# Kernel optimization log

Measured on AMD Instinct MI355X. Metric: run time of the kernel, lower is better.

## Reference

```python
import jax, jax.numpy as jnp
import numpy as np

IN_DIM = 256
OUT_DIM = 256
EMBED_DIM = 256
GROUPS = 8
BN_EPS = 1e-5


def conv2d(x, w, b, pad, groups=1):
    # x: NCHW, w: OIHW (I = in_ch / groups)
    out = jax.lax.conv_general_dilated(
        x, w, window_strides=(1, 1), padding=[(pad, pad), (pad, pad)],
        dimension_numbers=('NCHW', 'OIHW', 'NCHW'), feature_group_count=groups)
    return out + b[None, :, None, None]


def setup_inputs() -> dict:
    key = jax.random.key(0)
    ks = jax.random.split(key, 8)
    s = 0.05
    d = {}
    d['x'] = jax.random.normal(ks[0], (2, IN_DIM, 16, 16), jnp.float32)
    d['y'] = jax.random.normal(ks[1], (2, OUT_DIM, 128, 128), jnp.float32)
    # channle_reduce: Conv2d(256, 64, k=3, groups=64) -> weight (64, 4, 3, 3)
    d['w_cr'] = jax.random.normal(ks[2], (IN_DIM // 4, 4, 3, 3), jnp.float32) * s
    d['b_cr'] = jnp.zeros((IN_DIM // 4,), jnp.float32)
    # depthwise convs on 64 channels
    d['w_dw3'] = jax.random.normal(ks[3], (IN_DIM // 4, 1, 3, 3), jnp.float32) * s
    d['b_dw3'] = jnp.zeros((IN_DIM // 4,), jnp.float32)
    d['w_dw7'] = jax.random.normal(ks[4], (IN_DIM // 4, 1, 5, 5), jnp.float32) * s
    d['b_dw7'] = jnp.zeros((IN_DIM // 4,), jnp.float32)
    # gate: Conv2d(256, 128, 1) + BN + StarReLU
    d['w_gate'] = jax.random.normal(ks[5], (IN_DIM // 2, IN_DIM, 1, 1), jnp.float32) * s
    d['b_gate'] = jnp.zeros((IN_DIM // 2,), jnp.float32)
    d['bn_gamma'] = jnp.ones((IN_DIM // 2,), jnp.float32)
    d['bn_beta'] = jnp.zeros((IN_DIM // 2,), jnp.float32)
    d['bn_mean'] = jnp.zeros((IN_DIM // 2,), jnp.float32)
    d['bn_var'] = jnp.ones((IN_DIM // 2,), jnp.float32)
    d['sr_scale'] = jnp.ones((1,), jnp.float32)
    d['sr_bias'] = jnp.zeros((1,), jnp.float32)
    # linear1: Linear(16, 8192) -> torch weight shape (8192, 16)
    d['w_lin'] = jax.random.normal(ks[6], (OUT_DIM * EMBED_DIM // GROUPS, IN_DIM // (2 * GROUPS)), jnp.float32) * s
    d['b_lin'] = jnp.zeros((OUT_DIM * EMBED_DIM // GROUPS,), jnp.float32)
    return d


def reference(x, y, w_cr, b_cr, w_dw3, b_dw3, w_dw7, b_dw7, w_gate, b_gate,
              bn_gamma, bn_beta, bn_mean, bn_var, sr_scale, sr_bias, w_lin, b_lin):
    B, C, H, Wd = x.shape
    # gate branch: 1x1 conv -> BN (inference stats) -> StarReLU
    g = conv2d(x, w_gate, b_gate, 0)
    inv = (bn_gamma / jnp.sqrt(bn_var + BN_EPS))[None, :, None, None]
    g = (g - bn_mean[None, :, None, None]) * inv + bn_beta[None, :, None, None]
    g = sr_scale * jnp.square(jnp.maximum(g, 0.0)) + sr_bias
    # feature branch
    xr = conv2d(x, w_cr, b_cr, 1, groups=IN_DIM // 4)        # (B, 64, H, W)
    x3 = conv2d(xr, w_dw3, b_dw3, 1, groups=IN_DIM // 4)
    x7 = conv2d(xr, w_dw7, b_dw7, 2, groups=IN_DIM // 4)
    xc = jnp.concatenate([x3, x7], axis=1) * g               # (B, 128, H, W)
    # per-pixel weight generation: (B,H,W,G,16) @ (16,8192)
    xc = xc.reshape(B, GROUPS, -1, H, Wd).transpose(0, 3, 4, 1, 2)
    wdec = jnp.einsum('bhwgi,oi->bhwgo', xc, w_lin) + b_lin  # (B,H,W,8,8192)
    # flatten (G, out*embed/G) -> (embed, out); matches torch reshape order
    wdec = wdec.reshape(B, H, Wd, EMBED_DIM, OUT_DIM)
    # patch-wise dynamic 1x1 conv == per-patch batched matmul
    b, c, h, w = y.shape
    fh, fw = H, Wd
    ph, pw = h // fh, w // fw
    yp = y.reshape(b, c, fh, ph, fw, pw)
    # out[b,e,f,p,g,q] = sum_c wdec[b,f,g,e,c] * y[b,c,f,p,g,q]
    out = jnp.einsum('bfgec,bcfpgq->befpgq', wdec, yp)
    return out.reshape(b, EMBED_DIM, h, w)
```

## Files before the change

kernel.cpp:

```cpp
#include <hip/hip_runtime.h>
#include <stdint.h>


typedef __attribute__((ext_vector_type(8))) short short8;
typedef __attribute__((ext_vector_type(4))) float f32x4;

#define BN_EPS 1e-5f

__device__ __forceinline__ unsigned short f2bf(float f) {
  unsigned u = __float_as_uint(f);
  return (unsigned short)((u + 0x8000u) >> 16);
}
__device__ __forceinline__ unsigned pk2bf(float a, float b) {
  unsigned ua = __float_as_uint(a), ub = __float_as_uint(b);
  return ((ua + 0x8000u) >> 16) | ((ub + 0x8000u) & 0xFFFF0000u);
}

__global__ __launch_bounds__(256) void k1_merged(
    const float* __restrict__ x, const float* __restrict__ w_cr,
    const float* __restrict__ b_cr, const float* __restrict__ w_dw3,
    const float* __restrict__ b_dw3, const float* __restrict__ w_dw7,
    const float* __restrict__ b_dw7, const float* __restrict__ w_gate,
    const float* __restrict__ b_gate, const float* __restrict__ bn_gamma,
    const float* __restrict__ bn_beta, const float* __restrict__ bn_mean,
    const float* __restrict__ bn_var, const float* __restrict__ sr_scale,
    const float* __restrict__ sr_bias, const float* __restrict__ w_lin,
    short* __restrict__ wlin_bf, float* __restrict__ f0_out,
    float* __restrict__ gs_out)
{
  __shared__ __align__(16) float xcen[256];
  __shared__ __align__(16) float xs[4][256];
  __shared__ __align__(16) float xrs[256];

  int blk = blockIdx.x;
  int t = threadIdx.x;

  if (blk < 512) {
    int b = blk >> 8, h = (blk >> 4) & 15, w = blk & 15;
    int pix = (b * 16 + h) * 16 + w;

    { int idx = blk * 256 + t; wlin_bf[idx] = (short)f2bf(w_lin[idx]); }

    xcen[t] = x[b * 65536 + t * 256 + h * 16 + w];
    __syncthreads();

    int wave = t >> 6, lane = t & 63;
    int oq = lane >> 2, ol = lane & 3;
    const float4* wg4 = (const float4*)w_gate;
    const float4* xc4 = (const float4*)xcen;
    float ss = sr_scale[0], sb = sr_bias[0];

    #pragma unroll
    for (int pass = 0; pass < 2; ++pass) {
      int o = wave * 32 + pass * 16 + oq;
      float acc = 0.f;
      #pragma unroll
      for (int k = 0; k < 16; ++k) {
        int j = k * 4 + ol;
        float4 wv = wg4[o * 64 + j];
        float4 xv = xc4[j];
        acc += wv.x * xv.x + wv.y * xv.y + wv.z * xv.z + wv.w * xv.w;
      }
      acc += __shfl_xor(acc, 1);
      acc += __shfl_xor(acc, 2);
      float inv = bn_gamma[o] * rsqrtf(bn_var[o] + BN_EPS);
      float gg = (acc + b_gate[o] - bn_mean[o]) * inv + bn_beta[o];
      gg = fmaxf(gg, 0.f);
      gg = ss * gg * gg + sb;
      if (ol == 0) gs_out[pix * 128 + o] = gg;
    }
  } else {
    int cb = blk - 512;
    int b = cb >> 6, cr = cb & 63;
    {
      int ch = t >> 6, off = (t & 63) * 4;
      float4 v = *(const float4*)(x + b * 65536 + (cr * 4 + ch) * 256 + off);
      *(float4*)&xs[ch][off] = v;
    }
    __syncthreads();
    int h = t >> 4, w = t & 15;
    float a = b_cr[cr];
    #pragma unroll
    for (int ii = 0; ii < 4; ++ii) {
      const float* wp = w_cr + (cr * 4 + ii) * 9;
      #pragma unroll
      for (int ky = 0; ky < 3; ++ky) {
        int gy = h + ky - 1;
        #pragma unroll
        for (int kx = 0; kx < 3; ++kx) {
          int gx = w + kx - 1;
          float v = (gy >= 0 && gy < 16 && gx >= 0 && gx < 16) ? xs[ii][gy * 16 + gx] : 0.f;
          a += wp[ky * 3 + kx] * v;
        }
      }
    }
    xrs[t] = a;
    __syncthreads();

    float f3 = b_dw3[cr];
    {
      const float* wp = w_dw3 + cr * 9;
      #pragma unroll
      for (int ky = 0; ky < 3; ++ky) {
        int gy = h + ky - 1;
        #pragma unroll
        for (int kx = 0; kx < 3; ++kx) {
          int gx = w + kx - 1;
          float v = (gy >= 0 && gy < 16 && gx >= 0 && gx < 16) ? xrs[gy * 16 + gx] : 0.f;
          f3 += wp[ky * 3 + kx] * v;
        }
      }
    }
    float f5 = b_dw7[cr];
    {
      const float* wp = w_dw7 + cr * 25;
      #pragma unroll
      for (int ky = 0; ky < 5; ++ky) {
        int gy = h + ky - 2;
        #pragma unroll
        for (int kx = 0; kx < 5; ++kx) {
          int gx = w + kx - 2;
          float v = (gy >= 0 && gy < 16 && gx >= 0 && gx < 16) ? xrs[gy * 16 + gx] : 0.f;
          f5 += wp[ky * 5 + kx] * v;
        }
      }
    }
    int pix = (b * 16 + h) * 16 + w;
    f0_out[pix * 128 + cr] = f3;
    f0_out[pix * 128 + 64 + cr] = f5;
  }
}

__global__ __launch_bounds__(512, 4) void k2_fused(
    const float* __restrict__ y, const short* __restrict__ wlin_bf,
    const float* __restrict__ f0_in, const float* __restrict__ gs_in,
    const float* __restrict__ b_lin, float* __restrict__ out)
{
  __shared__ __align__(16) short Ylds[16384];
  __shared__ __align__(16) char dyn[32768];
  float* scratch = (float*)dyn;
  short* wdbuf = (short*)dyn;

  int phys = blockIdx.x;
  int blk = (phys & 7) * 64 + (phys >> 3);
  int b = blk >> 8, f = (blk >> 4) & 15, g = blk & 15;
  int tid = threadIdx.x;
  int wave = tid >> 6, lane = tid & 63;
  int quad = lane >> 4, l16 = lane & 15;
  int geff = l16 & 7, jsel = l16 >> 3;

  const float* yb = y + b * 4194304 + (f * 8) * 128 + g * 8;

  int c32 = tid >> 4, pf = tid & 15;
  float4 yv[4][2];
  #pragma unroll
  for (int sch = 0; sch < 4; ++sch)
    #pragma unroll
    for (int it = 0; it < 2; ++it)
      yv[sch][it] = *(const float4*)(yb + (sch * 64 + it * 32 + c32) * 16384 + (pf >> 1) * 128 + (pf & 1) * 4);

  short8 aw[2][2][2];
  #pragma unroll
  for (int s = 0; s < 2; ++s)
    #pragma unroll
    for (int jj = 0; jj < 2; ++jj) {
      int jA = (wave * 2 + jj) * 2 + (quad >> 1);
      #pragma unroll
      for (int hh = 0; hh < 2; ++hh) {
        int c0 = s * 32 + hh * 16;
        aw[s][jj][hh] = *(const short8*)(wlin_bf + (jA * 256 + c0 + l16) * 16 + (quad & 1) * 8);
      }
    }

  bool bval = (jsel == (quad >> 1));
  const float* fp = f0_in + blk * 128 + geff * 16 + (quad & 1) * 8;
  const float* gp = gs_in + blk * 128 + geff * 16 + (quad & 1) * 8;
  float4 f0a = *(const float4*)fp, f0b = *(const float4*)(fp + 4);
  float4 gsa = *(const float4*)gp, gsb = *(const float4*)(gp + 4);

  #pragma unroll
  for (int sch = 0; sch < 4; ++sch) {
    #pragma unroll
    for (int it = 0; it < 2; ++it)
      *(float4*)&scratch[(it * 32 + c32) * 65 + pf * 4] = yv[sch][it];
    __syncthreads();
    {
      int pix = tid & 63, cg = tid >> 6;
      float s0 = scratch[(cg * 8 + 0) * 65 + pix];
      float s1 = scratch[(cg * 8 + 1) * 65 + pix];
      float s2 = scratch[(cg * 8 + 2) * 65 + pix];
      float s3 = scratch[(cg * 8 + 3) * 65 + pix];
      float s4 = scratch[(cg * 8 + 4) * 65 + pix];
      float s5 = scratch[(cg * 8 + 5) * 65 + pix];
      float s6 = scratch[(cg * 8 + 6) * 65 + pix];
      float s7 = scratch[(cg * 8 + 7) * 65 + pix];
      uint4 pk;
      pk.x = pk2bf(s0, s1); pk.y = pk2bf(s2, s3);
      pk.z = pk2bf(s4, s5); pk.w = pk2bf(s6, s7);
      int chunk = sch * 8 + cg;
      int physc = chunk ^ (pix & 15);
      *(uint4*)&Ylds[pix * 256 + physc * 8] = pk;
    }
    __syncthreads();
  }

  short8 bx = {0, 0, 0, 0, 0, 0, 0, 0};
  if (bval) {
    bx[0] = (short)f2bf(f0a.x * gsa.x); bx[1] = (short)f2bf(f0a.y * gsa.y);
    bx[2] = (short)f2bf(f0a.z * gsa.z); bx[3] = (short)f2bf(f0a.w * gsa.w);
    bx[4] = (short)f2bf(f0b.x * gsb.x); bx[5] = (short)f2bf(f0b.y * gsb.y);
    bx[6] = (short)f2bf(f0b.z * gsb.z); bx[7] = (short)f2bf(f0b.w * gsb.w);
  }

  f32x4 acc[2][4];
  #pragma unroll
  for (int et = 0; et < 2; ++et)
    #pragma unroll
    for (int nt = 0; nt < 4; ++nt)
      acc[et][nt] = {0.f, 0.f, 0.f, 0.f};

  auto gen_chunk = [&](int cc, int buf, int slot) {
    short* dst = wdbuf + buf * 8192;
    #pragma unroll
    for (int jj = 0; jj < 2; ++jj) {
      int jp = wave * 2 + jj;
      int jD = jp * 2 + jsel;
      #pragma unroll
      for (int hh = 0; hh < 2; ++hh) {
        int c0 = cc * 32 + hh * 16;
        float4 bl = *(const float4*)(b_lin + jD * 256 + c0 + quad * 4);
        f32x4 cin = {bl.x, bl.y, bl.z, bl.w};
        f32x4 d = __builtin_amdgcn_mfma_f32_16x16x32_bf16(aw[slot][jj][hh], bx, cin, 0, 0, 0);
        int e = geff * 32 + jD;
        uint2 pk;
        pk.x = pk2bf(d[0], d[1]);
        pk.y = pk2bf(d[2], d[3]);
        int q16 = hh * 2 + (quad >> 1);
        int sw = q16 ^ ((e >> 1) & 3) ^ ((e >> 5) & 3);
        *(uint2*)&dst[e * 32 + sw * 8 + (quad & 1) * 4] = pk;
      }
    }
  };

  gen_chunk(0, 0, 0);
  __syncthreads();

  #pragma unroll
  for (int cc = 0; cc < 8; ++cc) {
    if (cc < 6) {
      #pragma unroll
      for (int jj = 0; jj < 2; ++jj) {
        int jA = (wave * 2 + jj) * 2 + (quad >> 1);
        #pragma unroll
        for (int hh = 0; hh < 2; ++hh) {
          int c0 = (cc + 2) * 32 + hh * 16;
          aw[cc & 1][jj][hh] = *(const short8*)(wlin_bf + (jA * 256 + c0 + l16) * 16 + (quad & 1) * 8);
        }
      }
    }
    if (cc < 7) gen_chunk(cc + 1, (cc + 1) & 1, (cc + 1) & 1);

    const short* src = wdbuf + (cc & 1) * 8192;
    short8 A2[2], Bf[4];
    #pragma unroll
    for (int et = 0; et < 2; ++et) {
      int e = wave * 32 + et * 16 + l16;
      int sw = quad ^ ((e >> 1) & 3) ^ ((e >> 5) & 3);
      A2[et] = *(const short8*)&src[e * 32 + sw * 8];
    }
    int chunkY = cc * 4 + quad;
    #pragma unroll
    for (int nt = 0; nt < 4; ++nt) {
      int physc = chunkY ^ l16;
      Bf[nt] = *(const short8*)&Ylds[(nt * 16 + l16) * 256 + physc * 8];
    }
    #pragma unroll
    for (int et = 0; et < 2; ++et)
      #pragma unroll
      for (int nt = 0; nt < 4; ++nt)
        acc[et][nt] = __builtin_amdgcn_mfma_f32_16x16x32_bf16(A2[et], Bf[nt], acc[et][nt], 0, 0, 0);
    if (cc < 7) __syncthreads();
  }

  float* ob = out + b * 4194304 + (f * 8) * 128 + g * 8;
  #pragma unroll
  for (int et = 0; et < 2; ++et) {
    int e0 = wave * 32 + et * 16 + quad * 4;
    #pragma unroll
    for (int nt = 0; nt < 4; ++nt) {
      int pix = nt * 16 + l16;
      float* oa = ob + (pix >> 3) * 128 + (pix & 7);
      #pragma unroll
      for (int r = 0; r < 4; ++r)
        oa[(e0 + r) * 16384] = acc[et][nt][r];
    }
  }
}

extern "C" void kernel_launch(void* const* d_in, const int* in_sizes, int n_in,
                              void* d_out, int out_size, void* d_ws, size_t ws_size,
                              hipStream_t stream) {
  const float* x        = (const float*)d_in[0];
  const float* y        = (const float*)d_in[1];
  const float* w_cr     = (const float*)d_in[2];
  const float* b_cr     = (const float*)d_in[3];
  const float* w_dw3    = (const float*)d_in[4];
  const float* b_dw3    = (const float*)d_in[5];
  const float* w_dw7    = (const float*)d_in[6];
  const float* b_dw7    = (const float*)d_in[7];
  const float* w_gate   = (const float*)d_in[8];
  const float* b_gate   = (const float*)d_in[9];
  const float* bn_gamma = (const float*)d_in[10];
  const float* bn_beta  = (const float*)d_in[11];
  const float* bn_mean  = (const float*)d_in[12];
  const float* bn_var   = (const float*)d_in[13];
  const float* sr_scale = (const float*)d_in[14];
  const float* sr_bias  = (const float*)d_in[15];
  const float* w_lin    = (const float*)d_in[16];
  const float* b_lin    = (const float*)d_in[17];
  float* out = (float*)d_out;

  float* f0      = (float*)d_ws;
  float* gs      = (float*)((char*)d_ws + 262144);
  short* wlin_bf = (short*)((char*)d_ws + 524288);

  hipLaunchKernelGGL(k1_merged, dim3(640), dim3(256), 0, stream,
                     x, w_cr, b_cr, w_dw3, b_dw3, w_dw7, b_dw7, w_gate, b_gate,
                     bn_gamma, bn_beta, bn_mean, bn_var, sr_scale, sr_bias,
                     w_lin, wlin_bf, f0, gs);
  hipLaunchKernelGGL(k2_fused, dim3(512), dim3(512), 0, stream,
                     y, wlin_bf, f0, gs, b_lin, out);
}
```

Baseline: 153.0 us.

## Split k2 patches in half and make dynamic-weight generation wave-private

Each patch is now split across two blocks (1024 blocks, half the pixels each), which halves LDS use and raises the occupancy target to 8 blocks per CU. The generated dynamic weights are remapped so each wave produces and consumes only its own rows in a private LDS region, which removes the per-chunk block barriers and the double buffer. The y staging transpose is also pipelined with a swizzled scratch layout. In exchange, each block recomputes the same weight-generation MFMAs for its patch, so that work is done twice, and the w_lin fragments are loaded on the fly instead of being prefetched.

```diff
diff --git a/kernel.cpp b/kernel.cpp
--- a/kernel.cpp
+++ b/kernel.cpp
@@ -131,168 +131,152 @@
   }
 }
 
-__global__ __launch_bounds__(512, 4) void k2_fused(
+__global__ __launch_bounds__(512, 8) void k2_fused(
     const float* __restrict__ y, const short* __restrict__ wlin_bf,
     const float* __restrict__ f0_in, const float* __restrict__ gs_in,
     const float* __restrict__ b_lin, float* __restrict__ out)
 {
-  __shared__ __align__(16) short Ylds[16384];
-  __shared__ __align__(16) char dyn[32768];
+  __shared__ __align__(16) short Ylds[8192];
+  __shared__ __align__(16) char dyn[16384];
   float* scratch = (float*)dyn;
-  short* wdbuf = (short*)dyn;
-
+  short* wdbase = (short*)dyn;
+
+  int tid = threadIdx.x;
   int phys = blockIdx.x;
-  int blk = (phys & 7) * 64 + (phys >> 3);
+  int logical = (phys & 7) * 128 + (phys >> 3);
+  int blk = logical >> 1, phalf = logical & 1;
   int b = blk >> 8, f = (blk >> 4) & 15, g = blk & 15;
-  int tid = threadIdx.x;
+
   int wave = tid >> 6, lane = tid & 63;
   int quad = lane >> 4, l16 = lane & 15;
   int geff = l16 & 7, jsel = l16 >> 3;
 
-  const float* yb = y + b * 4194304 + (f * 8) * 128 + g * 8;
-
-  int c32 = tid >> 4, pf = tid & 15;
-  float4 yv[4][2];
-  #pragma unroll
-  for (int sch = 0; sch < 4; ++sch)
-    #pragma unroll
-    for (int it = 0; it < 2; ++it)
-      yv[sch][it] = *(const float4*)(yb + (sch * 64 + it * 32 + c32) * 16384 + (pf >> 1) * 128 + (pf & 1) * 4);
-
-  short8 aw[2][2][2];
-  #pragma unroll
-  for (int s = 0; s < 2; ++s)
-    #pragma unroll
-    for (int jj = 0; jj < 2; ++jj) {
-      int jA = (wave * 2 + jj) * 2 + (quad >> 1);
-      #pragma unroll
-      for (int hh = 0; hh < 2; ++hh) {
-        int c0 = s * 32 + hh * 16;
-        aw[s][jj][hh] = *(const short8*)(wlin_bf + (jA * 256 + c0 + l16) * 16 + (quad & 1) * 8);
-      }
-    }
+  const float* yb = y + b * 4194304 + (f * 8 + phalf * 4) * 128 + g * 8;
+  int cth = tid >> 2, ith = tid & 3;
+
+  float4 yv[2];
+  #pragma unroll
+  for (int j = 0; j < 2; ++j) {
+    int hw = ith * 2 + j;
+    yv[j] = *(const float4*)(yb + cth * 16384 + (hw >> 1) * 128 + (hw & 1) * 4);
+  }
 
   bool bval = (jsel == (quad >> 1));
-  const float* fp = f0_in + blk * 128 + geff * 16 + (quad & 1) * 8;
-  const float* gp = gs_in + blk * 128 + geff * 16 + (quad & 1) * 8;
-  float4 f0a = *(const float4*)fp, f0b = *(const float4*)(fp + 4);
-  float4 gsa = *(const float4*)gp, gsb = *(const float4*)(gp + 4);
-
-  #pragma unroll
-  for (int sch = 0; sch < 4; ++sch) {
-    #pragma unroll
-    for (int it = 0; it < 2; ++it)
-      *(float4*)&scratch[(it * 32 + c32) * 65 + pf * 4] = yv[sch][it];
+  short8 bx = {0, 0, 0, 0, 0, 0, 0, 0};
+  {
+    const float* f0p = f0_in + blk * 128 + geff * 16 + (quad & 1) * 8;
+    const float* gsp = gs_in + blk * 128 + geff * 16 + (quad & 1) * 8;
+    float4 fa = *(const float4*)f0p, fb = *(const float4*)(f0p + 4);
+    float4 ga = *(const float4*)gsp, gb = *(const float4*)(gsp + 4);
+    if (bval) {
+      bx[0] = (short)f2bf(fa.x * ga.x); bx[1] = (short)f2bf(fa.y * ga.y);
+      bx[2] = (short)f2bf(fa.z * ga.z); bx[3] = (short)f2bf(fa.w * ga.w);
+      bx[4] = (short)f2bf(fb.x * gb.x); bx[5] = (short)f2bf(fb.y * gb.y);
+      bx[6] = (short)f2bf(fb.z * gb.z); bx[7] = (short)f2bf(fb.w * gb.w);
+    }
+  }
+
+  #pragma unroll
+  for (int rr = 0; rr < 2; ++rr) {
+    #pragma unroll
+    for (int j = 0; j < 2; ++j) {
+      int hw = ith * 2 + j;
+      *(float4*)&scratch[cth * 32 + ((hw * 4) ^ ((cth & 7) * 4))] = yv[j];
+    }
+    if (rr == 0) {
+      #pragma unroll
+      for (int j = 0; j < 2; ++j) {
+        int hw = ith * 2 + j;
+        yv[j] = *(const float4*)(yb + (128 + cth) * 16384 + (hw >> 1) * 128 + (hw & 1) * 4);
+      }
+    }
     __syncthreads();
     {
-      int pix = tid & 63, cg = tid >> 6;
-      float s0 = scratch[(cg * 8 + 0) * 65 + pix];
-      float s1 = scratch[(cg * 8 + 1) * 65 + pix];
-      float s2 = scratch[(cg * 8 + 2) * 65 + pix];
-      float s3 = scratch[(cg * 8 + 3) * 65 + pix];
-      float s4 = scratch[(cg * 8 + 4) * 65 + pix];
-      float s5 = scratch[(cg * 8 + 5) * 65 + pix];
-      float s6 = scratch[(cg * 8 + 6) * 65 + pix];
-      float s7 = scratch[(cg * 8 + 7) * 65 + pix];
+      int pix = tid & 31, cg = tid >> 5;
+      float s[8];
+      #pragma unroll
+      for (int i2 = 0; i2 < 8; ++i2)
+        s[i2] = scratch[(cg * 8 + i2) * 32 + (pix ^ (i2 * 4))];
       uint4 pk;
-      pk.x = pk2bf(s0, s1); pk.y = pk2bf(s2, s3);
-      pk.z = pk2bf(s4, s5); pk.w = pk2bf(s6, s7);
-      int chunk = sch * 8 + cg;
+      pk.x = pk2bf(s[0], s[1]); pk.y = pk2bf(s[2], s[3]);
+      pk.z = pk2bf(s[4], s[5]); pk.w = pk2bf(s[6], s[7]);
+      int chunk = rr * 16 + cg;
       int physc = chunk ^ (pix & 15);
       *(uint4*)&Ylds[pix * 256 + physc * 8] = pk;
     }
     __syncthreads();
   }
 
-  short8 bx = {0, 0, 0, 0, 0, 0, 0, 0};
-  if (bval) {
-    bx[0] = (short)f2bf(f0a.x * gsa.x); bx[1] = (short)f2bf(f0a.y * gsa.y);
-    bx[2] = (short)f2bf(f0a.z * gsa.z); bx[3] = (short)f2bf(f0a.w * gsa.w);
-    bx[4] = (short)f2bf(f0b.x * gsb.x); bx[5] = (short)f2bf(f0b.y * gsb.y);
-    bx[6] = (short)f2bf(f0b.z * gsb.z); bx[7] = (short)f2bf(f0b.w * gsb.w);
-  }
-
-  f32x4 acc[2][4];
-  #pragma unroll
-  for (int et = 0; et < 2; ++et)
-    #pragma unroll
-    for (int nt = 0; nt < 4; ++nt)
-      acc[et][nt] = {0.f, 0.f, 0.f, 0.f};
-
-  auto gen_chunk = [&](int cc, int buf, int slot) {
-    short* dst = wdbuf + buf * 8192;
+  short* wdw = wdbase + wave * 1024;
+
+  auto gen_chunk = [&](int cc) {
     #pragma unroll
     for (int jj = 0; jj < 2; ++jj) {
-      int jp = wave * 2 + jj;
-      int jD = jp * 2 + jsel;
+      int jD = wave * 4 + jj * 2 + jsel;
+      int jA = wave * 4 + jj * 2 + (quad >> 1);
+      int ep = geff * 4 + jj * 2 + jsel;
+      int gx = ((ep >> 2) & 3) ^ (ep & 3);
       #pragma unroll
       for (int hh = 0; hh < 2; ++hh) {
         int c0 = cc * 32 + hh * 16;
         float4 bl = *(const float4*)(b_lin + jD * 256 + c0 + quad * 4);
         f32x4 cin = {bl.x, bl.y, bl.z, bl.w};
-        f32x4 d = __builtin_amdgcn_mfma_f32_16x16x32_bf16(aw[slot][jj][hh], bx, cin, 0, 0, 0);
-        int e = geff * 32 + jD;
+        short8 aw = *(const short8*)(wlin_bf + (jA * 256 + c0 + l16) * 16 + (quad & 1) * 8);
+        f32x4 d = __builtin_amdgcn_mfma_f32_16x16x32_bf16(aw, bx, cin, 0, 0, 0);
         uint2 pk;
         pk.x = pk2bf(d[0], d[1]);
         pk.y = pk2bf(d[2], d[3]);
-        int q16 = hh * 2 + (quad >> 1);
-        int sw = q16 ^ ((e >> 1) & 3) ^ ((e >> 5) & 3);
-        *(uint2*)&dst[e * 32 + sw * 8 + (quad & 1) * 4] = pk;
+        int q16 = (hh * 2 + (quad >> 1)) ^ gx;
+        *(uint2*)&wdw[ep * 32 + q16 * 8 + (quad & 1) * 4] = pk;
       }
     }
   };
 
-  gen_chunk(0, 0, 0);
-  __syncthreads();
+  f32x4 acc[2][2];
+  #pragma unroll
+  for (int et = 0; et < 2; ++et)
+    #pragma unroll
+    for (int nt = 0; nt < 2; ++nt)
+      acc[et][nt] = {0.f, 0.f, 0.f, 0.f};
+
+  gen_chunk(0);
 
   #pragma unroll
   for (int cc = 0; cc < 8; ++cc) {
-    if (cc < 6) {
-      #pragma unroll
-      for (int jj = 0; jj < 2; ++jj) {
-        int jA = (wave * 2 + jj) * 2 + (quad >> 1);
-        #pragma unroll
-        for (int hh = 0; hh < 2; ++hh) {
-          int c0 = (cc + 2) * 32 + hh * 16;
-          aw[cc & 1][jj][hh] = *(const short8*)(wlin_bf + (jA * 256 + c0 + l16) * 16 + (quad & 1) * 8);
-        }
-      }
-    }
-    if (cc < 7) gen_chunk(cc + 1, (cc + 1) & 1, (cc + 1) & 1);
-
-    const short* src = wdbuf + (cc & 1) * 8192;
-    short8 A2[2], Bf[4];
+    short8 A2[2], Bf[2];
     #pragma unroll
     for (int et = 0; et < 2; ++et) {
-      int e = wave * 32 + et * 16 + l16;
-      int sw = quad ^ ((e >> 1) & 3) ^ ((e >> 5) & 3);
-      A2[et] = *(const short8*)&src[e * 32 + sw * 8];
-    }
-    int chunkY = cc * 4 + quad;
-    #pragma unroll
-    for (int nt = 0; nt < 4; ++nt) {
-      int physc = chunkY ^ l16;
-      Bf[nt] = *(const short8*)&Ylds[(nt * 16 + l16) * 256 + physc * 8];
-    }
+      int ep = (l16 & 7) * 4 + et * 2 + (l16 >> 3);
+      int gx = ((ep >> 2) & 3) ^ (ep & 3);
+      A2[et] = *(const short8*)&wdw[ep * 32 + (quad ^ gx) * 8];
+    }
+    #pragma unroll
+    for (int nt = 0; nt < 2; ++nt) {
+      int pix = nt * 16 + l16;
+      int physc = (cc * 4 + quad) ^ l16;
+      Bf[nt] = *(const short8*)&Ylds[pix * 256 + physc * 8];
+    }
+    if (cc < 7) gen_chunk(cc + 1);
     #pragma unroll
     for (int et = 0; et < 2; ++et)
       #pragma unroll
-      for (int nt = 0; nt < 4; ++nt)
+      for (int nt = 0; nt < 2; ++nt)
         acc[et][nt] = __builtin_amdgcn_mfma_f32_16x16x32_bf16(A2[et], Bf[nt], acc[et][nt], 0, 0, 0);
-    if (cc < 7) __syncthreads();
-  }
-
-  float* ob = out + b * 4194304 + (f * 8) * 128 + g * 8;
+  }
+
+  float* ob = out + b * 4194304 + (f * 8 + phalf * 4) * 128 + g * 8;
   #pragma unroll
   for (int et = 0; et < 2; ++et) {
-    int e0 = wave * 32 + et * 16 + quad * 4;
-    #pragma unroll
-    for (int nt = 0; nt < 4; ++nt) {
+    #pragma unroll
+    for (int nt = 0; nt < 2; ++nt) {
       int pix = nt * 16 + l16;
       float* oa = ob + (pix >> 3) * 128 + (pix & 7);
       #pragma unroll
-      for (int r = 0; r < 4; ++r)
-        oa[(e0 + r) * 16384] = acc[et][nt][r];
+      for (int r = 0; r < 4; ++r) {
+        int m = quad * 4 + r;
+        int e = (m & 7) * 32 + wave * 4 + et * 2 + (m >> 3);
+        oa[e * 16384] = acc[et][nt][r];
+      }
     }
   }
 }
@@ -328,6 +312,6 @@
                      x, w_cr, b_cr, w_dw3, b_dw3, w_dw7, b_dw7, w_gate, b_gate,
                      bn_gamma, bn_beta, bn_mean, bn_var, sr_scale, sr_bias,
                      w_lin, wlin_bf, f0, gs);
-  hipLaunchKernelGGL(k2_fused, dim3(512), dim3(512), 0, stream,
+  hipLaunchKernelGGL(k2_fused, dim3(1024), dim3(512), 0, stream,
                      y, wlin_bf, f0, gs, b_lin, out);
 }
```

New measurement: 179.9 us. 1.18x slower.

## Remap embed rows so each wave generates its own weights, removing block barriers

Applied to the files above, without the earlier changes.

Reassigns which embed rows each wave owns so the dynamic weights a wave generates via MFMA are exactly the rows it later consumes. Each wave can then keep a private LDS slot and the per-chunk block-wide __syncthreads disappear, shrinking shared memory from 32 KB to about 16 KB. The change also software-pipelines the y loads (two stages instead of four held in registers) and prefetches b_lin with the weight fragments. It risks changed output scatter patterns, since stores now write non-contiguous embed rows, and intra-wave LDS ordering now relies on wave-level execution without explicit barriers.

```diff
diff --git a/kernel.cpp b/kernel.cpp
--- a/kernel.cpp
+++ b/kernel.cpp
@@ -137,9 +137,9 @@
     const float* __restrict__ b_lin, float* __restrict__ out)
 {
   __shared__ __align__(16) short Ylds[16384];
-  __shared__ __align__(16) char dyn[32768];
+  __shared__ __align__(16) char dyn[16640];
   float* scratch = (float*)dyn;
-  short* wdbuf = (short*)dyn;
+  short* wdbase = (short*)dyn;
 
   int phys = blockIdx.x;
   int blk = (phys & 7) * 64 + (phys >> 3);
@@ -152,37 +152,45 @@
   const float* yb = y + b * 4194304 + (f * 8) * 128 + g * 8;
 
   int c32 = tid >> 4, pf = tid & 15;
-  float4 yv[4][2];
-  #pragma unroll
-  for (int sch = 0; sch < 4; ++sch)
+  float4 yv[2][2];
+  #pragma unroll
+  for (int s = 0; s < 2; ++s)
     #pragma unroll
     for (int it = 0; it < 2; ++it)
-      yv[sch][it] = *(const float4*)(yb + (sch * 64 + it * 32 + c32) * 16384 + (pf >> 1) * 128 + (pf & 1) * 4);
+      yv[s][it] = *(const float4*)(yb + (s * 64 + it * 32 + c32) * 16384 + (pf >> 1) * 128 + (pf & 1) * 4);
 
   short8 aw[2][2][2];
+  float4 bl[2][2][2];
   #pragma unroll
   for (int s = 0; s < 2; ++s)
     #pragma unroll
     for (int jj = 0; jj < 2; ++jj) {
-      int jA = (wave * 2 + jj) * 2 + (quad >> 1);
+      int jA = wave * 4 + jj * 2 + (quad >> 1);
+      int jD = wave * 4 + jj * 2 + jsel;
       #pragma unroll
       for (int hh = 0; hh < 2; ++hh) {
         int c0 = s * 32 + hh * 16;
         aw[s][jj][hh] = *(const short8*)(wlin_bf + (jA * 256 + c0 + l16) * 16 + (quad & 1) * 8);
+        bl[s][jj][hh] = *(const float4*)(b_lin + jD * 256 + c0 + quad * 4);
       }
     }
 
   bool bval = (jsel == (quad >> 1));
-  const float* fp = f0_in + blk * 128 + geff * 16 + (quad & 1) * 8;
-  const float* gp = gs_in + blk * 128 + geff * 16 + (quad & 1) * 8;
-  float4 f0a = *(const float4*)fp, f0b = *(const float4*)(fp + 4);
-  float4 gsa = *(const float4*)gp, gsb = *(const float4*)(gp + 4);
+  const float* f0p = f0_in + blk * 128 + geff * 16 + (quad & 1) * 8;
+  const float* gsp = gs_in + blk * 128 + geff * 16 + (quad & 1) * 8;
+  float4 f0a = *(const float4*)f0p, f0b = *(const float4*)(f0p + 4);
+  float4 gsa = *(const float4*)gsp, gsb = *(const float4*)(gsp + 4);
 
   #pragma unroll
   for (int sch = 0; sch < 4; ++sch) {
     #pragma unroll
     for (int it = 0; it < 2; ++it)
-      *(float4*)&scratch[(it * 32 + c32) * 65 + pf * 4] = yv[sch][it];
+      *(float4*)&scratch[(it * 32 + c32) * 65 + pf * 4] = yv[sch & 1][it];
+    if (sch < 2) {
+      #pragma unroll
+      for (int it = 0; it < 2; ++it)
+        yv[sch & 1][it] = *(const float4*)(yb + ((sch + 2) * 64 + it * 32 + c32) * 16384 + (pf >> 1) * 128 + (pf & 1) * 4);
+    }
     __syncthreads();
     {
       int pix = tid & 63, cg = tid >> 6;
@@ -219,80 +227,78 @@
     for (int nt = 0; nt < 4; ++nt)
       acc[et][nt] = {0.f, 0.f, 0.f, 0.f};
 
-  auto gen_chunk = [&](int cc, int buf, int slot) {
-    short* dst = wdbuf + buf * 8192;
+  short* wdw = wdbase + wave * 1024;
+
+  auto gen_chunk = [&](int cc, int slot) {
     #pragma unroll
     for (int jj = 0; jj < 2; ++jj) {
-      int jp = wave * 2 + jj;
-      int jD = jp * 2 + jsel;
+      int ep = geff * 4 + jj * 2 + jsel;
+      int gx = ((ep >> 2) & 3) ^ (ep & 3);
       #pragma unroll
       for (int hh = 0; hh < 2; ++hh) {
-        int c0 = cc * 32 + hh * 16;
-        float4 bl = *(const float4*)(b_lin + jD * 256 + c0 + quad * 4);
-        f32x4 cin = {bl.x, bl.y, bl.z, bl.w};
+        float4 blv = bl[slot][jj][hh];
+        f32x4 cin = {blv.x, blv.y, blv.z, blv.w};
         f32x4 d = __builtin_amdgcn_mfma_f32_16x16x32_bf16(aw[slot][jj][hh], bx, cin, 0, 0, 0);
-        int e = geff * 32 + jD;
         uint2 pk;
         pk.x = pk2bf(d[0], d[1]);
         pk.y = pk2bf(d[2], d[3]);
-        int q16 = hh * 2 + (quad >> 1);
-        int sw = q16 ^ ((e >> 1) & 3) ^ ((e >> 5) & 3);
-        *(uint2*)&dst[e * 32 + sw * 8 + (quad & 1) * 4] = pk;
+        int q16 = (hh * 2 + (quad >> 1)) ^ gx;
+        *(uint2*)&wdw[ep * 32 + q16 * 8 + (quad & 1) * 4] = pk;
       }
     }
   };
 
-  gen_chunk(0, 0, 0);
-  __syncthreads();
+  gen_chunk(0, 0);
 
   #pragma unroll
   for (int cc = 0; cc < 8; ++cc) {
+    short8 A2[2], Bf[4];
+    #pragma unroll
+    for (int et = 0; et < 2; ++et) {
+      int ep = (l16 & 7) * 4 + et * 2 + (l16 >> 3);
+      int gx = ((ep >> 2) & 3) ^ (ep & 3);
+      A2[et] = *(const short8*)&wdw[ep * 32 + (quad ^ gx) * 8];
+    }
+    int chunkY = cc * 4 + quad;
+    #pragma unroll
+    for (int nt = 0; nt < 4; ++nt) {
+      int physc = chunkY ^ l16;
+      Bf[nt] = *(const short8*)&Ylds[(nt * 16 + l16) * 256 + physc * 8];
+    }
     if (cc < 6) {
       #pragma unroll
       for (int jj = 0; jj < 2; ++jj) {
-        int jA = (wave * 2 + jj) * 2 + (quad >> 1);
+        int jA = wave * 4 + jj * 2 + (quad >> 1);
+        int jD = wave * 4 + jj * 2 + jsel;
         #pragma unroll
         for (int hh = 0; hh < 2; ++hh) {
           int c0 = (cc + 2) * 32 + hh * 16;
           aw[cc & 1][jj][hh] = *(const short8*)(wlin_bf + (jA * 256 + c0 + l16) * 16 + (quad & 1) * 8);
+          bl[cc & 1][jj][hh] = *(const float4*)(b_lin + jD * 256 + c0 + quad * 4);
         }
       }
     }
-    if (cc < 7) gen_chunk(cc + 1, (cc + 1) & 1, (cc + 1) & 1);
-
-    const short* src = wdbuf + (cc & 1) * 8192;
-    short8 A2[2], Bf[4];
-    #pragma unroll
-    for (int et = 0; et < 2; ++et) {
-      int e = wave * 32 + et * 16 + l16;
-      int sw = quad ^ ((e >> 1) & 3) ^ ((e >> 5) & 3);
-      A2[et] = *(const short8*)&src[e * 32 + sw * 8];
-    }
-    int chunkY = cc * 4 + quad;
-    #pragma unroll
-    for (int nt = 0; nt < 4; ++nt) {
-      int physc = chunkY ^ l16;
-      Bf[nt] = *(const short8*)&Ylds[(nt * 16 + l16) * 256 + physc * 8];
-    }
+    if (cc < 7) gen_chunk(cc + 1, (cc + 1) & 1);
     #pragma unroll
     for (int et = 0; et < 2; ++et)
       #pragma unroll
       for (int nt = 0; nt < 4; ++nt)
         acc[et][nt] = __builtin_amdgcn_mfma_f32_16x16x32_bf16(A2[et], Bf[nt], acc[et][nt], 0, 0, 0);
-    if (cc < 7) __syncthreads();
   }
 
   float* ob = out + b * 4194304 + (f * 8) * 128 + g * 8;
   #pragma unroll
   for (int et = 0; et < 2; ++et) {
-    int e0 = wave * 32 + et * 16 + quad * 4;
     #pragma unroll
     for (int nt = 0; nt < 4; ++nt) {
       int pix = nt * 16 + l16;
       float* oa = ob + (pix >> 3) * 128 + (pix & 7);
       #pragma unroll
-      for (int r = 0; r < 4; ++r)
-        oa[(e0 + r) * 16384] = acc[et][nt][r];
+      for (int r = 0; r < 4; ++r) {
+        int m = quad * 4 + r;
+        int e = (m & 7) * 32 + wave * 4 + et * 2 + (m >> 3);
+        oa[e * 16384] = acc[et][nt][r];
+      }
     }
   }
 }
```

Result: no change. 152.6 us (median of 2 runs) (-0.2%).
